# Kernel tuning notes

Measured on AMD Instinct MI355X. Metric: run time of the kernel, lower is better.

Reference implementation:

```python
import jax, jax.numpy as jnp
import numpy as np

N_SAMPLES, N_TIME, N_FEAT = 64, 4, 64
N_ENTITIES = 10000
D = N_TIME * N_FEAT  # 256
K = 10


def setup_inputs() -> dict:
    key = jax.random.key(0)
    k1, k2 = jax.random.split(key)
    query = jax.random.uniform(k1, (N_SAMPLES, N_TIME, N_FEAT), dtype=jnp.float32)
    # module state: self.enity_info, flattened view must be [n_entities, D]
    enity_info = jax.random.uniform(k2, (N_ENTITIES, D), dtype=jnp.float32)
    return {"query": query, "enity_info": enity_info, "k": K}


def reference(query, enity_info, k):
    n_samples = query.shape[0]
    q = query.reshape(n_samples, -1)                 # [n, d]
    e = enity_info.reshape(enity_info.shape[0], -1)  # [m, d]
    # pairwise Jaccard: sum(min) / sum(max) over feature dim
    inter = jnp.sum(jnp.minimum(q[:, None, :], e[None, :, :]), axis=2)  # [n, m]
    union = jnp.sum(jnp.maximum(q[:, None, :], e[None, :, :]), axis=2)  # [n, m]
    jaccard = inter / union                                             # [n, m]
    # torch.topk largest=True, sorted=True -> lax.top_k (descending)
    _, top_idx = jax.lax.top_k(jaccard, k)
    # torch.topk largest=False, sorted=True -> ascending smallest: top_k of negated
    _, bot_idx = jax.lax.top_k(-jaccard, k)
    return top_idx, bot_idx
```

## Files before the change

### kernel.cpp

```cpp
#include <hip/hip_runtime.h>
#include <math.h>
#include <limits.h>

#define NQ     64
#define NE     10000
#define K      10
#define NSTRIP 250
#define EPB    40
#define TPB    512
#define EPP    5
#define SLOT   11
#define SCALE  8388608.0f

__device__ __forceinline__ bool better_top(double v, int i, double v2, int i2) {
    return (v > v2) || (v == v2 && i < i2);
}

__device__ __forceinline__ void merge_slots16(double* Mv, unsigned short* Mi, int A, int B) {
    double ov[K]; unsigned short oi[K];
    int a = 0, b = 0;
#pragma unroll
    for (int o = 0; o < K; ++o) {
        double va = Mv[A * SLOT + a]; int ia = Mi[A * SLOT + a];
        double vb = Mv[B * SLOT + b]; int ib = Mi[B * SLOT + b];
        bool pick = better_top(va, ia, vb, ib);
        ov[o] = pick ? va : vb;
        oi[o] = (unsigned short)(pick ? ia : ib);
        if (pick) ++a; else ++b;
    }
#pragma unroll
    for (int o = 0; o < K; ++o) { Mv[A * SLOT + o] = ov[o]; Mi[A * SLOT + o] = oi[o]; }
}


#define CSWAP(v, ii, A, B)                                                 \
    {                                                                      \
        bool c_ = better_top(v[B], ii[B], v[A], ii[A]);                    \
        double tv_ = c_ ? v[B] : v[A]; double uv_ = c_ ? v[A] : v[B];      \
        int    ti_ = c_ ? ii[B] : ii[A]; int ui_ = c_ ? ii[A] : ii[B];     \
        v[A] = tv_; v[B] = uv_; ii[A] = ti_; ii[B] = ui_;                  \
    }
#define SORT5(v, ii)            \
    CSWAP(v, ii, 0, 1) CSWAP(v, ii, 3, 4) CSWAP(v, ii, 2, 4) \
    CSWAP(v, ii, 2, 3) CSWAP(v, ii, 0, 3) CSWAP(v, ii, 0, 2) \
    CSWAP(v, ii, 1, 4) CSWAP(v, ii, 1, 3) CSWAP(v, ii, 1, 2)

__global__ __launch_bounds__(256) void ent_sums(const float* __restrict__ E,
                                                unsigned* __restrict__ Se) {
    const int w = threadIdx.x >> 6, l = threadIdx.x & 63;
    const int j = blockIdx.x * 4 + w;
    float4 v = reinterpret_cast<const float4*>(E)[(size_t)j * 64 + l];
    unsigned s = (unsigned)(v.x * SCALE) + (unsigned)(v.y * SCALE)
               + (unsigned)(v.z * SCALE) + (unsigned)(v.w * SCALE);
#pragma unroll
    for (int m = 1; m < 64; m <<= 1) s += (unsigned)__shfl_xor((int)s, m, 64);
    if (l == 0) Se[j] = s;
}

__global__ __launch_bounds__(TPB, 2) void jac_part(
        const float* __restrict__ Q, const float* __restrict__ E,
        const unsigned* __restrict__ Se,
        double* __restrict__ pvT, double* __restrict__ pvB,
        int* __restrict__ piT, int* __restrict__ piB) {
    __shared__ uint4 QT[2048];
    __shared__ uint4 EB[8][EPP][65];

    const int t    = threadIdx.x;
    const int l    = t & 63;
    const int w    = t >> 6;
    const int q    = l >> 1;
    const int sub  = l & 1;
    const int strip = blockIdx.x >> 1;
    const int qbase = (blockIdx.x & 1) * 32;
    const int q64  = qbase + q;

    unsigned* SqP = (unsigned*)&EB[0][0][0];
    {
        const int sq = t >> 4, c = t & 15;
        unsigned acc = 0;
#pragma unroll
        for (int r = 0; r < 4; ++r) {
            const int gg = c + 16 * r;
            float4 v = reinterpret_cast<const float4*>(Q)[(qbase + sq) * 64 + gg];
            uint4 u;
            u.x = (unsigned)(v.x * SCALE); u.y = (unsigned)(v.y * SCALE);
            u.z = (unsigned)(v.z * SCALE); u.w = (unsigned)(v.w * SCALE);
            QT[(gg & 31) * 64 + 2 * sq + (gg >> 5)] = u;
            acc += u.x + u.y + u.z + u.w;
        }
        SqP[t] = acc;
    }
    __syncthreads();
    unsigned Sq = 0;
#pragma unroll
    for (int pp = 0; pp < 16; ++pp) Sq += SqP[q * 16 + ((pp + q) & 15)];
    __syncthreads();

    const int jb = strip * EPB;
    const float4* E4 = (const float4*)E;

#pragma unroll
    for (int s = 0; s < EPP; ++s) {
        float4 er = E4[(size_t)(jb + w + 8 * s) * 64 + l];
        uint4 eu;
        eu.x = (unsigned)(er.x * SCALE); eu.y = (unsigned)(er.y * SCALE);
        eu.z = (unsigned)(er.z * SCALE); eu.w = (unsigned)(er.w * SCALE);
        EB[w][s][l + (l >> 5)] = eu;
    }
    unsigned se[EPP];
#pragma unroll
    for (int s = 0; s < EPP; ++s) se[s] = Se[jb + w + 8 * s];

    const uint4* ebr = &EB[w][0][sub * 33];
    unsigned a0[EPP], a1[EPP];
#pragma unroll
    for (int s = 0; s < EPP; ++s) { a0[s] = 0; a1[s] = 0; }

#pragma unroll 4
    for (int g = 0; g < 32; ++g) {
        uint4 qv = QT[g * 64 + l];
#pragma unroll
        for (int s = 0; s < EPP; ++s) {
            uint4 ev = ebr[s * 65 + g];
            a0[s] += min(qv.x, ev.x) + min(qv.y, ev.y);
            a1[s] += min(qv.z, ev.z) + min(qv.w, ev.w);
        }
    }

    double av[EPP]; int ai[EPP]; double bv[EPP]; int bi[EPP];
#pragma unroll
    for (int s = 0; s < EPP; ++s) {
        unsigned ih = a0[s] + a1[s];
        unsigned inter = ih + (unsigned)__shfl_xor((int)ih, 1, 64);
        unsigned uni   = Sq + se[s] - inter;
        double jac = (double)inter / (double)uni;
        av[s] = jac;  ai[s] = jb + w + 8 * s;
        bv[s] = -jac; bi[s] = ai[s];
    }
    SORT5(av, ai)
    SORT5(bv, bi)

    __syncthreads();
    double*         MvA = (double*)&QT[0];
    unsigned short* MiA = (unsigned short*)((char*)&QT[0] + 22528);
    double*         MvB = (double*)&EB[0][0][0];
    unsigned short* MiB = (unsigned short*)((char*)&EB[0][0][0] + 22528);
    double*         Mv  = sub ? MvB : MvA;
    unsigned short* Mi  = sub ? MiB : MiA;
    const int slot = w * 32 + q;

#pragma unroll
    for (int o = 0; o < EPP; ++o) {
        Mv[slot * SLOT + o] = sub ? bv[o] : av[o];
        Mi[slot * SLOT + o] = (unsigned short)(sub ? bi[o] : ai[o]);
    }
#pragma unroll
    for (int o = EPP; o < K; ++o) { Mv[slot * SLOT + o] = -INFINITY; Mi[slot * SLOT + o] = 0xFFFFu; }
    __syncthreads();

    for (int s = 4; s >= 1; s >>= 1) {
        if (w < s) merge_slots16(Mv, Mi, w * 32 + q, (w + s) * 32 + q);
        if (s > 1) __syncthreads();
    }
    if (w == 0) {
        const size_t off = ((size_t)q64 * NSTRIP + strip) * K;
        double* pv = sub ? pvB : pvT;
        int*    pi = sub ? piB : piT;
#pragma unroll
        for (int o = 0; o < K; ++o) { pv[off + o] = Mv[q * SLOT + o]; pi[off + o] = (int)Mi[q * SLOT + o]; }
    }
}

__global__ __launch_bounds__(256) void final_extract(
        const double* __restrict__ pvT, const double* __restrict__ pvB,
        const int* __restrict__ piT, const int* __restrict__ piB,
        int* __restrict__ out) {
    __shared__ double Lv[NSTRIP * K];
    __shared__ int    Li[NSTRIP * K];
    __shared__ double Wv[4];
    __shared__ int    Wi[4], Wo[4];
    __shared__ int    res[K];

    const int b   = blockIdx.x;
    const int q   = b >> 1;
    const bool top = (b & 1) == 0;
    const int t   = threadIdx.x;
    const int l   = t & 63;
    const int w   = t >> 6;

    const double* V = (top ? pvT : pvB) + (size_t)q * NSTRIP * K;
    const int*    I = (top ? piT : piB) + (size_t)q * NSTRIP * K;

    for (int i = t; i < NSTRIP * K; i += 256) {
        Lv[i] = V[i];
        Li[i] = I[i];
    }
    __syncthreads();

    int h = 0;
    double hv = (t < NSTRIP) ? Lv[t * K] : -INFINITY;
    int    hi = (t < NSTRIP) ? Li[t * K] : INT_MAX;

    for (int r = 0; r < K; ++r) {
        double v = hv; int idx = hi; int own = t;
#pragma unroll
        for (int m = 1; m < 64; m <<= 1) {
            double ov = __shfl_xor(v, m, 64);
            int    oi = __shfl_xor(idx, m, 64);
            int    oo = __shfl_xor(own, m, 64);
            if (better_top(ov, oi, v, idx)) { v = ov; idx = oi; own = oo; }
        }
        if (l == 0) { Wv[w] = v; Wi[w] = idx; Wo[w] = own; }
        __syncthreads();
        double gv = Wv[0]; int gi = Wi[0], go = Wo[0];
#pragma unroll
        for (int ww = 1; ww < 4; ++ww)
            if (better_top(Wv[ww], Wi[ww], gv, gi)) { gv = Wv[ww]; gi = Wi[ww]; go = Wo[ww]; }
        if (t == go) {
            ++h;
            bool ok = h < K;
            hv = ok ? Lv[t * K + h] : -INFINITY;
            hi = ok ? Li[t * K + h] : INT_MAX;
        }
        if (t == 0) res[r] = gi;
        __syncthreads();
    }

    if (t < K) out[(top ? 0 : NQ * K) + q * K + t] = res[t];
}

extern "C" void kernel_launch(void* const* d_in, const int* in_sizes, int n_in,
                              void* d_out, int out_size, void* d_ws, size_t ws_size,
                              hipStream_t stream) {
    const float* Q = (const float*)d_in[0];
    const float* E = (const float*)d_in[1];
    int* out = (int*)d_out;

    char* ws = (char*)d_ws;
    unsigned* Se  = (unsigned*)(ws);
    double*   pvT = (double*)(ws + 40960);
    double*   pvB = (double*)(ws + 1320960);
    int*      piT = (int*)   (ws + 2600960);
    int*      piB = (int*)   (ws + 3240960);

    hipLaunchKernelGGL(ent_sums, dim3(NE / 4), dim3(256), 0, stream, E, Se);
    hipLaunchKernelGGL(jac_part, dim3(NSTRIP * 2), dim3(TPB), 0, stream,
                       Q, E, Se, pvT, pvB, piT, piB);
    hipLaunchKernelGGL(final_extract, dim3(NQ * 2), dim3(256), 0, stream,
                       pvT, pvB, piT, piB, out);
}
```

Measured before the change: 45.16 us.

## Assign one query per lane and broadcast entity values via readlane

Restructures jac_part so each 256-thread block covers 20 entities across all 64 queries. Each lane owns one query, and the entity features held in registers are broadcast with readlane instead of being staged in shared memory, which also removes the pair-lane shuffle. The query sums are now computed inline in the loop. The number of partial top-k lists doubles to 500 per query, so final_extract first does a pairwise merge while loading. The cost is more global partial writes and scalar readlane traffic in the inner loop, in return for less LDS traffic.

```diff
diff --git a/kernel.cpp b/kernel.cpp
--- a/kernel.cpp
+++ b/kernel.cpp
@@ -5,10 +5,11 @@
 #define NQ     64
 #define NE     10000
 #define K      10
-#define NSTRIP 250
-#define EPB    40
-#define TPB    512
-#define EPP    5
+#define NBLK   500
+#define EPB    20
+#define TPB    256
+#define NWAVE  4
+#define EPW    5
 #define SLOT   11
 #define SCALE  8388608.0f
 
@@ -32,7 +33,6 @@
     for (int o = 0; o < K; ++o) { Mv[A * SLOT + o] = ov[o]; Mi[A * SLOT + o] = oi[o]; }
 }
 
-
 #define CSWAP(v, ii, A, B)                                                 \
     {                                                                      \
         bool c_ = better_top(v[B], ii[B], v[A], ii[A]);                    \
@@ -62,80 +62,70 @@
         const unsigned* __restrict__ Se,
         double* __restrict__ pvT, double* __restrict__ pvB,
         int* __restrict__ piT, int* __restrict__ piB) {
-    __shared__ uint4 QT[2048];
-    __shared__ uint4 EB[8][EPP][65];
-
-    const int t    = threadIdx.x;
-    const int l    = t & 63;
-    const int w    = t >> 6;
-    const int q    = l >> 1;
-    const int sub  = l & 1;
-    const int strip = blockIdx.x >> 1;
-    const int qbase = (blockIdx.x & 1) * 32;
-    const int q64  = qbase + q;
-
-    unsigned* SqP = (unsigned*)&EB[0][0][0];
-    {
-        const int sq = t >> 4, c = t & 15;
-        unsigned acc = 0;
-#pragma unroll
-        for (int r = 0; r < 4; ++r) {
-            const int gg = c + 16 * r;
-            float4 v = reinterpret_cast<const float4*>(Q)[(qbase + sq) * 64 + gg];
-            uint4 u;
-            u.x = (unsigned)(v.x * SCALE); u.y = (unsigned)(v.y * SCALE);
-            u.z = (unsigned)(v.z * SCALE); u.w = (unsigned)(v.w * SCALE);
-            QT[(gg & 31) * 64 + 2 * sq + (gg >> 5)] = u;
-            acc += u.x + u.y + u.z + u.w;
-        }
-        SqP[t] = acc;
-    }
-    __syncthreads();
-    unsigned Sq = 0;
-#pragma unroll
-    for (int pp = 0; pp < 16; ++pp) Sq += SqP[q * 16 + ((pp + q) & 15)];
-    __syncthreads();
-
-    const int jb = strip * EPB;
+    __shared__ uint4 QT[64 * 65];
+
+    const int t = threadIdx.x;
+    const int l = t & 63;
+    const int w = t >> 6;
+    const int b = blockIdx.x;
+    const int ebase = b * EPB + w * EPW;
+
     const float4* E4 = (const float4*)E;
-
-#pragma unroll
-    for (int s = 0; s < EPP; ++s) {
-        float4 er = E4[(size_t)(jb + w + 8 * s) * 64 + l];
-        uint4 eu;
-        eu.x = (unsigned)(er.x * SCALE); eu.y = (unsigned)(er.y * SCALE);
-        eu.z = (unsigned)(er.z * SCALE); eu.w = (unsigned)(er.w * SCALE);
-        EB[w][s][l + (l >> 5)] = eu;
-    }
-    unsigned se[EPP];
-#pragma unroll
-    for (int s = 0; s < EPP; ++s) se[s] = Se[jb + w + 8 * s];
-
-    const uint4* ebr = &EB[w][0][sub * 33];
-    unsigned a0[EPP], a1[EPP];
-#pragma unroll
-    for (int s = 0; s < EPP; ++s) { a0[s] = 0; a1[s] = 0; }
-
-#pragma unroll 4
-    for (int g = 0; g < 32; ++g) {
-        uint4 qv = QT[g * 64 + l];
-#pragma unroll
-        for (int s = 0; s < EPP; ++s) {
-            uint4 ev = ebr[s * 65 + g];
-            a0[s] += min(qv.x, ev.x) + min(qv.y, ev.y);
-            a1[s] += min(qv.z, ev.z) + min(qv.w, ev.w);
-        }
-    }
-
-    double av[EPP]; int ai[EPP]; double bv[EPP]; int bi[EPP];
-#pragma unroll
-    for (int s = 0; s < EPP; ++s) {
-        unsigned ih = a0[s] + a1[s];
-        unsigned inter = ih + (unsigned)__shfl_xor((int)ih, 1, 64);
-        unsigned uni   = Sq + se[s] - inter;
+    const float4* Q4 = (const float4*)Q;
+
+    float4 er[EPW];
+#pragma unroll
+    for (int s = 0; s < EPW; ++s) er[s] = E4[(size_t)(ebase + s) * 64 + l];
+    unsigned se[EPW];
+#pragma unroll
+    for (int s = 0; s < EPW; ++s) se[s] = Se[ebase + s];
+
+#pragma unroll
+    for (int it = 0; it < 16; ++it) {
+        const int f = t + TPB * it;
+        float4 v = Q4[f];
+        uint4 u;
+        u.x = (unsigned)(v.x * SCALE); u.y = (unsigned)(v.y * SCALE);
+        u.z = (unsigned)(v.z * SCALE); u.w = (unsigned)(v.w * SCALE);
+        QT[(f & 63) * 65 + (f >> 6)] = u;
+    }
+
+    uint4 eu[EPW];
+#pragma unroll
+    for (int s = 0; s < EPW; ++s) {
+        eu[s].x = (unsigned)(er[s].x * SCALE); eu[s].y = (unsigned)(er[s].y * SCALE);
+        eu[s].z = (unsigned)(er[s].z * SCALE); eu[s].w = (unsigned)(er[s].w * SCALE);
+    }
+    __syncthreads();
+
+    unsigned a0[EPW], a1[EPW];
+#pragma unroll
+    for (int s = 0; s < EPW; ++s) { a0[s] = 0; a1[s] = 0; }
+    unsigned sq = 0;
+
+#pragma unroll 8
+    for (int g = 0; g < 64; ++g) {
+        uint4 qv = QT[g * 65 + l];
+        sq += (qv.x + qv.y) + (qv.z + qv.w);
+#pragma unroll
+        for (int s = 0; s < EPW; ++s) {
+            unsigned ex = (unsigned)__builtin_amdgcn_readlane((int)eu[s].x, g);
+            unsigned ey = (unsigned)__builtin_amdgcn_readlane((int)eu[s].y, g);
+            unsigned ez = (unsigned)__builtin_amdgcn_readlane((int)eu[s].z, g);
+            unsigned ew = (unsigned)__builtin_amdgcn_readlane((int)eu[s].w, g);
+            a0[s] += min(qv.x, ex) + min(qv.y, ey);
+            a1[s] += min(qv.z, ez) + min(qv.w, ew);
+        }
+    }
+
+    double av[EPW]; int ai[EPW]; double bv[EPW]; int bi[EPW];
+#pragma unroll
+    for (int s = 0; s < EPW; ++s) {
+        unsigned inter = a0[s] + a1[s];
+        unsigned uni   = sq + se[s] - inter;
         double jac = (double)inter / (double)uni;
-        av[s] = jac;  ai[s] = jb + w + 8 * s;
-        bv[s] = -jac; bi[s] = ai[s];
+        av[s] = jac;  ai[s] = ebase + s;
+        bv[s] = -jac; bi[s] = ebase + s;
     }
     SORT5(av, ai)
     SORT5(bv, bi)
@@ -143,31 +133,36 @@
     __syncthreads();
     double*         MvA = (double*)&QT[0];
     unsigned short* MiA = (unsigned short*)((char*)&QT[0] + 22528);
-    double*         MvB = (double*)&EB[0][0][0];
-    unsigned short* MiB = (unsigned short*)((char*)&EB[0][0][0] + 22528);
-    double*         Mv  = sub ? MvB : MvA;
-    unsigned short* Mi  = sub ? MiB : MiA;
-    const int slot = w * 32 + q;
-
-#pragma unroll
-    for (int o = 0; o < EPP; ++o) {
-        Mv[slot * SLOT + o] = sub ? bv[o] : av[o];
-        Mi[slot * SLOT + o] = (unsigned short)(sub ? bi[o] : ai[o]);
-    }
-#pragma unroll
-    for (int o = EPP; o < K; ++o) { Mv[slot * SLOT + o] = -INFINITY; Mi[slot * SLOT + o] = 0xFFFFu; }
-    __syncthreads();
-
-    for (int s = 4; s >= 1; s >>= 1) {
-        if (w < s) merge_slots16(Mv, Mi, w * 32 + q, (w + s) * 32 + q);
-        if (s > 1) __syncthreads();
-    }
+    double*         MvB = (double*)((char*)&QT[0] + 28160);
+    unsigned short* MiB = (unsigned short*)((char*)&QT[0] + 50688);
+    const int slot = w * 64 + l;
+
+#pragma unroll
+    for (int o = 0; o < EPW; ++o) {
+        MvA[slot * SLOT + o] = av[o]; MiA[slot * SLOT + o] = (unsigned short)ai[o];
+        MvB[slot * SLOT + o] = bv[o]; MiB[slot * SLOT + o] = (unsigned short)bi[o];
+    }
+#pragma unroll
+    for (int o = EPW; o < K; ++o) {
+        MvA[slot * SLOT + o] = -INFINITY; MiA[slot * SLOT + o] = 0xFFFFu;
+        MvB[slot * SLOT + o] = -INFINITY; MiB[slot * SLOT + o] = 0xFFFFu;
+    }
+    __syncthreads();
+
+    if (w < 2) {
+        merge_slots16(MvA, MiA, w * 64 + l, (w + 2) * 64 + l);
+        merge_slots16(MvB, MiB, w * 64 + l, (w + 2) * 64 + l);
+    }
+    __syncthreads();
     if (w == 0) {
-        const size_t off = ((size_t)q64 * NSTRIP + strip) * K;
-        double* pv = sub ? pvB : pvT;
-        int*    pi = sub ? piB : piT;
-#pragma unroll
-        for (int o = 0; o < K; ++o) { pv[off + o] = Mv[q * SLOT + o]; pi[off + o] = (int)Mi[q * SLOT + o]; }
+        merge_slots16(MvA, MiA, l, 64 + l);
+        merge_slots16(MvB, MiB, l, 64 + l);
+        const size_t off = ((size_t)l * NBLK + b) * K;
+#pragma unroll
+        for (int o = 0; o < K; ++o) {
+            pvT[off + o] = MvA[l * SLOT + o]; piT[off + o] = (int)MiA[l * SLOT + o];
+            pvB[off + o] = MvB[l * SLOT + o]; piB[off + o] = (int)MiB[l * SLOT + o];
+        }
     }
 }
 
@@ -175,31 +170,48 @@
         const double* __restrict__ pvT, const double* __restrict__ pvB,
         const int* __restrict__ piT, const int* __restrict__ piB,
         int* __restrict__ out) {
-    __shared__ double Lv[NSTRIP * K];
-    __shared__ int    Li[NSTRIP * K];
+    __shared__ double Lv[256 * K];
+    __shared__ int    Li[256 * K];
     __shared__ double Wv[4];
     __shared__ int    Wi[4], Wo[4];
     __shared__ int    res[K];
 
-    const int b   = blockIdx.x;
-    const int q   = b >> 1;
-    const bool top = (b & 1) == 0;
+    const int bid = blockIdx.x;
+    const int q   = bid >> 1;
+    const bool top = (bid & 1) == 0;
     const int t   = threadIdx.x;
     const int l   = t & 63;
     const int w   = t >> 6;
 
-    const double* V = (top ? pvT : pvB) + (size_t)q * NSTRIP * K;
-    const int*    I = (top ? piT : piB) + (size_t)q * NSTRIP * K;
-
-    for (int i = t; i < NSTRIP * K; i += 256) {
-        Lv[i] = V[i];
-        Li[i] = I[i];
+    const double* V = (top ? pvT : pvB) + (size_t)q * NBLK * K;
+    const int*    I = (top ? piT : piB) + (size_t)q * NBLK * K;
+
+    {
+        double ov[K]; int oi[K];
+        const int lb = t + 256;
+        if (lb < NBLK) {
+            int a = 0, bn = 0;
+            const size_t sa = (size_t)t * K, sb = (size_t)lb * K;
+#pragma unroll
+            for (int o = 0; o < K; ++o) {
+                double va = V[sa + a];  int ia = I[sa + a];
+                double vb = V[sb + bn]; int ib = I[sb + bn];
+                bool pick = better_top(va, ia, vb, ib);
+                ov[o] = pick ? va : vb; oi[o] = pick ? ia : ib;
+                if (pick) ++a; else ++bn;
+            }
+        } else {
+#pragma unroll
+            for (int o = 0; o < K; ++o) { ov[o] = V[(size_t)t * K + o]; oi[o] = I[(size_t)t * K + o]; }
+        }
+#pragma unroll
+        for (int o = 0; o < K; ++o) { Lv[t * K + o] = ov[o]; Li[t * K + o] = oi[o]; }
     }
     __syncthreads();
 
     int h = 0;
-    double hv = (t < NSTRIP) ? Lv[t * K] : -INFINITY;
-    int    hi = (t < NSTRIP) ? Li[t * K] : INT_MAX;
+    double hv = Lv[t * K];
+    int    hi = Li[t * K];
 
     for (int r = 0; r < K; ++r) {
         double v = hv; int idx = hi; int own = t;
@@ -239,12 +251,12 @@
     char* ws = (char*)d_ws;
     unsigned* Se  = (unsigned*)(ws);
     double*   pvT = (double*)(ws + 40960);
-    double*   pvB = (double*)(ws + 1320960);
-    int*      piT = (int*)   (ws + 2600960);
-    int*      piB = (int*)   (ws + 3240960);
+    double*   pvB = (double*)(ws + 2600960);
+    int*      piT = (int*)   (ws + 5160960);
+    int*      piB = (int*)   (ws + 6440960);
 
     hipLaunchKernelGGL(ent_sums, dim3(NE / 4), dim3(256), 0, stream, E, Se);
-    hipLaunchKernelGGL(jac_part, dim3(NSTRIP * 2), dim3(TPB), 0, stream,
+    hipLaunchKernelGGL(jac_part, dim3(NBLK), dim3(TPB), 0, stream,
                        Q, E, Se, pvT, pvB, piT, piB);
     hipLaunchKernelGGL(final_extract, dim3(NQ * 2), dim3(256), 0, stream,
                        pvT, pvB, piT, piB, out);
```

Result: slower. 53.33 us (+18.1%).
